# Kernel optimization log

Hardware: AMD Instinct MI355X
Metric: run time of the kernel (lower is better)

The kernel has to match this reference:

```python
import jax, jax.numpy as jnp
import numpy as np

N = 50000
E = 800000
D_IN = 256
HID = 64
HEADS = 4
OUT = 86
EPS_BN = 1e-5
NEG_SLOPE = 0.2


def setup_inputs() -> dict:
    key = jax.random.key(0)
    ks = jax.random.split(key, 16)
    HC = HEADS * HID
    inp = {
        "x": jax.random.normal(ks[0], (N, D_IN), jnp.float32),
        "edge_index": jax.random.randint(ks[1], (2, E), 0, N, jnp.int64),
        # GATConv 1: in=D_IN, out per head=HID, concat=True
        "W1": jax.random.normal(ks[2], (D_IN, HC), jnp.float32) * (1.0 / np.sqrt(D_IN)),
        "att_src1": jax.random.normal(ks[3], (HEADS, HID), jnp.float32) * 0.1,
        "att_dst1": jax.random.normal(ks[4], (HEADS, HID), jnp.float32) * 0.1,
        "b1": jnp.zeros((HC,), jnp.float32),
        # GATConv 2: in=HC, out per head=HID, concat=False (mean over heads)
        "W2": jax.random.normal(ks[5], (HC, HC), jnp.float32) * (1.0 / np.sqrt(HC)),
        "att_src2": jax.random.normal(ks[6], (HEADS, HID), jnp.float32) * 0.1,
        "att_dst2": jax.random.normal(ks[7], (HEADS, HID), jnp.float32) * 0.1,
        "b2": jnp.zeros((HID,), jnp.float32),
        # BatchNorms
        "g1": jnp.ones((HC,), jnp.float32),
        "be1": jnp.zeros((HC,), jnp.float32),
        "g2": jnp.ones((HID,), jnp.float32),
        "be2": jnp.zeros((HID,), jnp.float32),
        # PReLU (single shared weight, torch default init 0.25)
        "prelu_w": jnp.asarray(0.25, jnp.float32),
        # final Linear
        "fcW": jax.random.normal(ks[8], (HID, OUT), jnp.float32) * (1.0 / np.sqrt(HID)),
        "fcb": jnp.zeros((OUT,), jnp.float32),
    }
    return inp


def _gat_conv(x, src, dst, W, att_src, att_dst, bias, concat):
    # PyG GATConv forward (dropout inactive in eval mode).
    n = x.shape[0]
    H, C = att_src.shape
    h = (x @ W).reshape(n, H, C)                      # [N,H,C]
    a_s = jnp.sum(h * att_src[None], axis=-1)         # [N,H]
    a_d = jnp.sum(h * att_dst[None], axis=-1)         # [N,H]
    logits = jax.nn.leaky_relu(a_s[src] + a_d[dst], NEG_SLOPE)  # [E,H]
    # segment softmax over edges grouped by destination node
    m = jax.ops.segment_max(logits, dst, num_segments=n)        # [N,H]
    e = jnp.exp(logits - m[dst])
    s = jax.ops.segment_sum(e, dst, num_segments=n)             # [N,H]
    alpha = e / (s[dst] + 1e-16)                                # [E,H]
    msg = h[src] * alpha[:, :, None]                            # [E,H,C]
    out = jax.ops.segment_sum(msg, dst, num_segments=n)         # [N,H,C]
    if concat:
        return out.reshape(n, H * C) + bias
    return out.mean(axis=1) + bias


def _batch_norm(x, gamma, beta):
    mu = x.mean(axis=0)
    var = x.var(axis=0)
    return gamma * (x - mu) * jax.lax.rsqrt(var + EPS_BN) + beta


def reference(x, edge_index, W1, att_src1, att_dst1, b1, W2, att_src2, att_dst2, b2,
              g1, be1, g2, be2, prelu_w, fcW, fcb):
    n = x.shape[0]
    # GATConv default add_self_loops=True
    loops = jnp.arange(n, dtype=edge_index.dtype)
    src = jnp.concatenate([edge_index[0], loops])
    dst = jnp.concatenate([edge_index[1], loops])

    h = _gat_conv(x, src, dst, W1, att_src1, att_dst1, b1, concat=True)
    h = _batch_norm(h, g1, be1)
    h = jnp.where(h >= 0, h, prelu_w * h)             # PReLU
    # dropout: identity (eval)
    h = _gat_conv(h, src, dst, W2, att_src2, att_dst2, b2, concat=False)
    h = _batch_norm(h, g2, be2)
    h = jax.nn.elu(h)
    return h @ fcW + fcb
```

## Files before the change

### kernel.cpp

```cpp
#include <hip/hip_runtime.h>
#include <math.h>

#define LEAKY 0.2f

typedef __attribute__((ext_vector_type(8))) short short8;
typedef __attribute__((ext_vector_type(4))) float f32x4;

__device__ __forceinline__ float leaky02(float z) { return z >= 0.f ? z : LEAKY * z; }
__device__ __forceinline__ unsigned short f2bf(float f) {
  unsigned u = __float_as_uint(f);
  unsigned r = u + 0x7fffu + ((u >> 16) & 1u);
  return (unsigned short)(r >> 16);
}
__device__ __forceinline__ float bflo(unsigned u) { return __uint_as_float(u << 16); }
__device__ __forceinline__ float bfhi(unsigned u) { return __uint_as_float(u & 0xffff0000u); }

__global__ void count_kernel(const int* __restrict__ ei, int* __restrict__ cnt, int E, int N) {
  int e = blockIdx.x * 256 + threadIdx.x;
  int EP = E + N;
  if (e >= EP) return;
  int d = (e < E) ? ei[E + e] : (e - E);
  atomicAdd(&cnt[d], 1);
}

__global__ __launch_bounds__(256) void scan1_kernel(const int* __restrict__ cnt,
                                                    int* __restrict__ bsums, int n) {
  int i = blockIdx.x * 256 + threadIdx.x;
  int v = (i < n) ? cnt[i] : 0;
  int lane = threadIdx.x & 63, wv = threadIdx.x >> 6;
#pragma unroll
  for (int off = 32; off; off >>= 1) v += __shfl_xor(v, off);
  __shared__ int w[4];
  if (lane == 0) w[wv] = v;
  __syncthreads();
  if (threadIdx.x == 0) bsums[blockIdx.x] = w[0] + w[1] + w[2] + w[3];
}

__global__ __launch_bounds__(256) void scan2_kernel(int* __restrict__ bsums, int nb) {
  int tid = threadIdx.x;
  int lane = tid & 63, wv = tid >> 6;
  int v = (tid < nb) ? bsums[tid] : 0;
  int x = v;
#pragma unroll
  for (int off = 1; off < 64; off <<= 1) {
    int t = __shfl_up(x, off);
    if (lane >= off) x += t;
  }
  __shared__ int ws[4];
  if (lane == 63) ws[wv] = x;
  __syncthreads();
  int woff = 0;
#pragma unroll
  for (int w = 0; w < 4; ++w) if (w < wv) woff += ws[w];
  if (tid < nb) bsums[tid] = x + woff - v;
}

__global__ __launch_bounds__(256) void scan3_kernel(const int* __restrict__ cnt,
                                                    const int* __restrict__ boff,
                                                    int* __restrict__ rowptr,
                                                    int* __restrict__ cursor, int n) {
  int i = blockIdx.x * 256 + threadIdx.x;
  int tid = threadIdx.x, lane = tid & 63, wv = tid >> 6;
  int v = (i < n) ? cnt[i] : 0;
  int x = v;
#pragma unroll
  for (int off = 1; off < 64; off <<= 1) {
    int t = __shfl_up(x, off);
    if (lane >= off) x += t;
  }
  __shared__ int ws[4];
  if (lane == 63) ws[wv] = x;
  __syncthreads();
  int woff = 0;
#pragma unroll
  for (int w = 0; w < 4; ++w) if (w < wv) woff += ws[w];
  int incl = x + woff;
  int base = boff[blockIdx.x];
  if (i < n) {
    rowptr[i + 1] = base + incl;
    cursor[i] = base + incl - v;
  }
  if (i == 0) rowptr[0] = 0;
}

__global__ void fill_kernel(const int* __restrict__ ei, int* __restrict__ cursor,
                            int* __restrict__ srcs, int E, int N) {
  int e = blockIdx.x * 256 + threadIdx.x;
  int EP = E + N;
  if (e >= EP) return;
  int s, d;
  if (e < E) { s = ei[e]; d = ei[E + e]; } else { s = e - E; d = s; }
  int slot = atomicAdd(&cursor[d], 1);
  srcs[slot] = s;
}

__global__ void convw_kernel(const float* __restrict__ W1, const float* __restrict__ W2,
                             unsigned short* __restrict__ Wt1, unsigned short* __restrict__ Wt2) {
  int idx = blockIdx.x * 256 + threadIdx.x;
  const float* W;
  unsigned short* Wt;
  if (idx < 65536) { W = W1; Wt = Wt1; } else { W = W2; Wt = Wt2; idx -= 65536; }
  int c = idx >> 8, k = idx & 255;
  Wt[c * 256 + k] = f2bf(W[k * 256 + c]);
}

template <bool BF16A>
__global__ __launch_bounds__(512) void gemm_kernel(const void* __restrict__ Av,
                                                   const unsigned short* __restrict__ Wt,
                                                   unsigned short* __restrict__ Hout, int M,
                                                   const float* __restrict__ bnsc,
                                                   const float* __restrict__ bnsh,
                                                   const float* __restrict__ pwp,
                                                   const float* __restrict__ att_s,
                                                   const float* __restrict__ att_d,
                                                   float* __restrict__ as_o,
                                                   float* __restrict__ ad_o) {
  __shared__ unsigned short As[128][40];
  __shared__ unsigned short Bs[256][40];
  int tid = threadIdx.x;
  int bm = blockIdx.x * 128;
  int l = tid & 63, wv = tid >> 6;
  int wm = wv >> 2, wn = wv & 3;
  int lr = l & 15, lk = l >> 4;
  f32x4 acc[4][4] = {};
  float pws = pwp ? pwp[0] : 0.f;

  for (int k0 = 0; k0 < 256; k0 += 32) {
#pragma unroll
    for (int it = 0; it < 2; ++it) {
      int i = tid + it * 512;
      int row = i >> 3, kk = (i & 7) * 4;
      int gr = bm + row;
      float v0, v1, v2, v3;
      if (BF16A) {
        uint2 u = make_uint2(0, 0);
        if (gr < M) u = *(const uint2*)((const unsigned short*)Av + (size_t)gr * 256 + k0 + kk);
        v0 = bflo(u.x); v1 = bfhi(u.x); v2 = bflo(u.y); v3 = bfhi(u.y);
      } else {
        float4 va = make_float4(0.f, 0.f, 0.f, 0.f);
        if (gr < M) va = *(const float4*)((const float*)Av + (size_t)gr * 256 + k0 + kk);
        v0 = va.x; v1 = va.y; v2 = va.z; v3 = va.w;
      }
      if (bnsc) {
        float4 sc = *(const float4*)&bnsc[k0 + kk];
        float4 sh = *(const float4*)&bnsh[k0 + kk];
        v0 = fmaf(v0, sc.x, sh.x); v1 = fmaf(v1, sc.y, sh.y);
        v2 = fmaf(v2, sc.z, sh.z); v3 = fmaf(v3, sc.w, sh.w);
        v0 = v0 >= 0.f ? v0 : v0 * pws; v1 = v1 >= 0.f ? v1 : v1 * pws;
        v2 = v2 >= 0.f ? v2 : v2 * pws; v3 = v3 >= 0.f ? v3 : v3 * pws;
      }
      ushort4 u4;
      u4.x = f2bf(v0); u4.y = f2bf(v1); u4.z = f2bf(v2); u4.w = f2bf(v3);
      *(ushort4*)&As[row][kk] = u4;
    }
#pragma unroll
    for (int it = 0; it < 4; ++it) {
      int i = tid + it * 512;
      int c = i >> 3, kk = (i & 7) * 4;
      *(ushort4*)&Bs[c][kk] = *(const ushort4*)&Wt[(size_t)c * 256 + k0 + kk];
    }
    __syncthreads();
    short8 af[4], bfr[4];
#pragma unroll
    for (int mt = 0; mt < 4; ++mt) af[mt] = *(const short8*)&As[wm * 64 + mt * 16 + lr][lk * 8];
#pragma unroll
    for (int nt = 0; nt < 4; ++nt) bfr[nt] = *(const short8*)&Bs[wn * 64 + nt * 16 + lr][lk * 8];
#pragma unroll
    for (int mt = 0; mt < 4; ++mt)
#pragma unroll
      for (int nt = 0; nt < 4; ++nt)
        acc[mt][nt] = __builtin_amdgcn_mfma_f32_16x16x32_bf16(af[mt], bfr[nt], acc[mt][nt], 0, 0, 0);
    __syncthreads();
  }
  float asv[4], adv[4];
#pragma unroll
  for (int nt = 0; nt < 4; ++nt) {
    int gc = wn * 64 + nt * 16 + lr;
    asv[nt] = att_s[gc];
    adv[nt] = att_d[gc];
  }
#pragma unroll
  for (int mt = 0; mt < 4; ++mt) {
#pragma unroll
    for (int r = 0; r < 4; ++r) {
      int gr = bm + wm * 64 + mt * 16 + lk * 4 + r;
      float ps = acc[mt][0][r] * asv[0] + acc[mt][1][r] * asv[1] +
                 acc[mt][2][r] * asv[2] + acc[mt][3][r] * asv[3];
      float pd = acc[mt][0][r] * adv[0] + acc[mt][1][r] * adv[1] +
                 acc[mt][2][r] * adv[2] + acc[mt][3][r] * adv[3];
#pragma unroll
      for (int off = 1; off < 16; off <<= 1) {
        ps += __shfl_xor(ps, off);
        pd += __shfl_xor(pd, off);
      }
      if (lr == 0 && gr < M) {
        as_o[gr * 4 + wn] = ps;
        ad_o[gr * 4 + wn] = pd;
      }
      if (gr < M) {
#pragma unroll
        for (int nt = 0; nt < 4; ++nt)
          Hout[(size_t)gr * 256 + wn * 64 + nt * 16 + lr] = f2bf(acc[mt][nt][r]);
      }
    }
  }
}

__global__ __launch_bounds__(256) void agg_kernel(const unsigned short* __restrict__ h,
                                                  const float* __restrict__ as_,
                                                  const float* __restrict__ ad_,
                                                  const int* __restrict__ rowptr,
                                                  const int* __restrict__ srcs,
                                                  const float* __restrict__ bias,
                                                  unsigned short* __restrict__ out_bf,
                                                  float* __restrict__ out_f,
                                                  int N, int concat) {
  int l = threadIdx.x & 63;
  int n = blockIdx.x * 4 + (threadIdx.x >> 6);
  if (n >= N) return;
  int e0 = rowptr[n], e1 = rowptr[n + 1];
  int deg = e1 - e0;
  int hh = l >> 4, le = l & 15;
  float adh = ad_[n * 4 + hh];
  float a0 = 0.f, a1 = 0.f, a2 = 0.f, a3 = 0.f;

  if (deg <= 64) {
    int sidx[4];
    float lg[4];
#pragma unroll
    for (int t = 0; t < 4; ++t) {
      int j = e0 + le + 16 * t;
      if (j < e1) {
        int s = srcs[j];
        sidx[t] = s;
        lg[t] = leaky02(as_[s * 4 + hh] + adh);
      } else {
        sidx[t] = 0;
        lg[t] = -1e30f;
      }
    }
    float mx = fmaxf(fmaxf(lg[0], lg[1]), fmaxf(lg[2], lg[3]));
#pragma unroll
    for (int off = 1; off < 16; off <<= 1) mx = fmaxf(mx, __shfl_xor(mx, off));
    float ex[4];
    float sm = 0.f;
#pragma unroll
    for (int t = 0; t < 4; ++t) {
      ex[t] = (lg[t] > -1e29f) ? __expf(lg[t] - mx) : 0.f;
      sm += ex[t];
    }
#pragma unroll
    for (int off = 1; off < 16; off <<= 1) sm += __shfl_xor(sm, off);
    float inv = 1.f / (sm + 1e-16f);
    int hsel = hh << 4;
#pragma unroll
    for (int t = 0; t < 4; ++t) {
      int base = e0 + 16 * t;
      if (base >= e1) continue;
      int cntc = min(16, e1 - base);
#pragma unroll 4
      for (int q = 0; q < cntc; ++q) {
        int s = __shfl(sidx[t], q);
        float al = __shfl(ex[t], q + hsel) * inv;
        uint2 hv = *(const uint2*)&h[(size_t)s * 256 + l * 4];
        a0 = fmaf(bflo(hv.x), al, a0);
        a1 = fmaf(bfhi(hv.x), al, a1);
        a2 = fmaf(bflo(hv.y), al, a2);
        a3 = fmaf(bfhi(hv.y), al, a3);
      }
    }
  } else {
    float ad4[4] = {ad_[n * 4], ad_[n * 4 + 1], ad_[n * 4 + 2], ad_[n * 4 + 3]};
    float mx[4] = {-1e30f, -1e30f, -1e30f, -1e30f};
    for (int j = e0 + l; j < e1; j += 64) {
      int s = srcs[j];
      float4 av = *(const float4*)&as_[s * 4];
      mx[0] = fmaxf(mx[0], leaky02(av.x + ad4[0]));
      mx[1] = fmaxf(mx[1], leaky02(av.y + ad4[1]));
      mx[2] = fmaxf(mx[2], leaky02(av.z + ad4[2]));
      mx[3] = fmaxf(mx[3], leaky02(av.w + ad4[3]));
    }
#pragma unroll
    for (int off = 32; off; off >>= 1) {
      mx[0] = fmaxf(mx[0], __shfl_xor(mx[0], off));
      mx[1] = fmaxf(mx[1], __shfl_xor(mx[1], off));
      mx[2] = fmaxf(mx[2], __shfl_xor(mx[2], off));
      mx[3] = fmaxf(mx[3], __shfl_xor(mx[3], off));
    }
    float sm[4] = {0.f, 0.f, 0.f, 0.f};
    for (int j = e0 + l; j < e1; j += 64) {
      int s = srcs[j];
      float4 av = *(const float4*)&as_[s * 4];
      sm[0] += __expf(leaky02(av.x + ad4[0]) - mx[0]);
      sm[1] += __expf(leaky02(av.y + ad4[1]) - mx[1]);
      sm[2] += __expf(leaky02(av.z + ad4[2]) - mx[2]);
      sm[3] += __expf(leaky02(av.w + ad4[3]) - mx[3]);
    }
#pragma unroll
    for (int off = 32; off; off >>= 1) {
      sm[0] += __shfl_xor(sm[0], off);
      sm[1] += __shfl_xor(sm[1], off);
      sm[2] += __shfl_xor(sm[2], off);
      sm[3] += __shfl_xor(sm[3], off);
    }
    float mh = hh == 0 ? mx[0] : hh == 1 ? mx[1] : hh == 2 ? mx[2] : mx[3];
    float sh = hh == 0 ? sm[0] : hh == 1 ? sm[1] : hh == 2 ? sm[2] : sm[3];
    float inv = 1.f / (sh + 1e-16f);
    int j = e0;
    for (; j + 2 <= e1; j += 2) {
      int s0 = srcs[j], s1 = srcs[j + 1];
      float x0 = as_[s0 * 4 + hh], x1 = as_[s1 * 4 + hh];
      uint2 h0 = *(const uint2*)&h[(size_t)s0 * 256 + l * 4];
      uint2 h1 = *(const uint2*)&h[(size_t)s1 * 256 + l * 4];
      float al0 = __expf(leaky02(x0 + adh) - mh) * inv;
      float al1 = __expf(leaky02(x1 + adh) - mh) * inv;
      a0 = fmaf(bflo(h0.x), al0, a0); a1 = fmaf(bfhi(h0.x), al0, a1);
      a2 = fmaf(bflo(h0.y), al0, a2); a3 = fmaf(bfhi(h0.y), al0, a3);
      a0 = fmaf(bflo(h1.x), al1, a0); a1 = fmaf(bfhi(h1.x), al1, a1);
      a2 = fmaf(bflo(h1.y), al1, a2); a3 = fmaf(bfhi(h1.y), al1, a3);
    }
    for (; j < e1; ++j) {
      int s = srcs[j];
      float al = __expf(leaky02(as_[s * 4 + hh] + adh) - mh) * inv;
      uint2 hv = *(const uint2*)&h[(size_t)s * 256 + l * 4];
      a0 = fmaf(bflo(hv.x), al, a0); a1 = fmaf(bfhi(hv.x), al, a1);
      a2 = fmaf(bflo(hv.y), al, a2); a3 = fmaf(bfhi(hv.y), al, a3);
    }
  }

  if (concat) {
    float4 b4 = *(const float4*)&bias[l * 4];
    ushort4 o;
    o.x = f2bf(a0 + b4.x); o.y = f2bf(a1 + b4.y);
    o.z = f2bf(a2 + b4.z); o.w = f2bf(a3 + b4.w);
    *(ushort4*)&out_bf[(size_t)n * 256 + l * 4] = o;
  } else {
    a0 += __shfl_xor(a0, 16); a0 += __shfl_xor(a0, 32);
    a1 += __shfl_xor(a1, 16); a1 += __shfl_xor(a1, 32);
    a2 += __shfl_xor(a2, 16); a2 += __shfl_xor(a2, 32);
    a3 += __shfl_xor(a3, 16); a3 += __shfl_xor(a3, 32);
    if (l < 16) {
      float4 b4 = *(const float4*)&bias[l * 4];
      float4 o = make_float4(0.25f * a0 + b4.x, 0.25f * a1 + b4.y,
                             0.25f * a2 + b4.z, 0.25f * a3 + b4.w);
      *(float4*)&out_f[(size_t)n * 64 + l * 4] = o;
    }
  }
}

__global__ __launch_bounds__(256) void bnstats_bf16_kernel(const unsigned short* __restrict__ x,
                                                           float* __restrict__ sum,
                                                           float* __restrict__ ss, int N) {
  int tid = threadIdx.x;
  int c = (tid & 127) * 2;
  int r = blockIdx.x * 2 + (tid >> 7);
  int stride = gridDim.x * 2;
  float a0 = 0.f, b0 = 0.f, a1 = 0.f, b1 = 0.f;
  for (; r < N; r += stride) {
    unsigned u = *(const unsigned*)&x[(size_t)r * 256 + c];
    float v0 = bflo(u), v1 = bfhi(u);
    a0 += v0; b0 += v0 * v0;
    a1 += v1; b1 += v1 * v1;
  }
  atomicAdd(&sum[c], a0); atomicAdd(&ss[c], b0);
  atomicAdd(&sum[c + 1], a1); atomicAdd(&ss[c + 1], b1);
}

__global__ __launch_bounds__(256) void bnstats_kernel(const float* __restrict__ x,
                                                      float* __restrict__ sum, float* __restrict__ ss,
                                                      int N, int C) {
  int tid = threadIdx.x;
  int f = tid % C;
  int rpb = 256 / C;
  int r = blockIdx.x * rpb + tid / C;
  int stride = gridDim.x * rpb;
  float a = 0.f, b = 0.f;
  for (; r < N; r += stride) {
    float v = x[(size_t)r * C + f];
    a += v;
    b += v * v;
  }
  atomicAdd(&sum[f], a);
  atomicAdd(&ss[f], b);
}

__global__ void bnfinalize_kernel(const float* __restrict__ sum, const float* __restrict__ ss,
                                  const float* __restrict__ gamma, const float* __restrict__ beta,
                                  float* __restrict__ scale, float* __restrict__ shift, int N, int C) {
  int f = threadIdx.x;
  if (f >= C) return;
  float mu = sum[f] / (float)N;
  float var = ss[f] / (float)N - mu * mu;
  float sc = gamma[f] * rsqrtf(var + 1e-5f);
  scale[f] = sc;
  shift[f] = beta[f] - mu * sc;
}

__global__ __launch_bounds__(256) void fc_kernel(const float* __restrict__ x,
                                                 const float* __restrict__ sc, const float* __restrict__ sh,
                                                 const float* __restrict__ W, const float* __restrict__ b,
                                                 float* __restrict__ out, int N) {
  __shared__ float ws[64 * 86];
  __shared__ float xs[32 * 64];
  int tid = threadIdx.x;
  for (int i = tid; i < 64 * 86; i += 256) ws[i] = W[i];
  int n0 = blockIdx.x * 32;
  for (int i = tid; i < 32 * 64; i += 256) {
    int n = n0 + (i >> 6), c = i & 63;
    float v = (n < N) ? x[(size_t)n * 64 + c] : 0.f;
    v = fmaf(v, sc[c], sh[c]);
    xs[i] = v > 0.f ? v : expm1f(v);
  }
  __syncthreads();
  for (int idx = tid; idx < 32 * 86; idx += 256) {
    int nl = idx / 86, o = idx % 86;
    int n = n0 + nl;
    if (n >= N) continue;
    float acc = b[o];
    const float* xr = &xs[nl * 64];
#pragma unroll 8
    for (int k = 0; k < 64; ++k) acc = fmaf(xr[k], ws[k * 86 + o], acc);
    out[(size_t)n * 86 + o] = acc;
  }
}

extern "C" void kernel_launch(void* const* d_in, const int* in_sizes, int n_in,
                              void* d_out, int out_size, void* d_ws, size_t ws_size,
                              hipStream_t stream) {
  const float* x    = (const float*)d_in[0];
  const int*   ei   = (const int*)d_in[1];
  const float* W1   = (const float*)d_in[2];
  const float* asw1 = (const float*)d_in[3];
  const float* adw1 = (const float*)d_in[4];
  const float* b1   = (const float*)d_in[5];
  const float* W2   = (const float*)d_in[6];
  const float* asw2 = (const float*)d_in[7];
  const float* adw2 = (const float*)d_in[8];
  const float* b2   = (const float*)d_in[9];
  const float* g1   = (const float*)d_in[10];
  const float* be1  = (const float*)d_in[11];
  const float* g2   = (const float*)d_in[12];
  const float* be2  = (const float*)d_in[13];
  const float* pw   = (const float*)d_in[14];
  const float* fcW  = (const float*)d_in[15];
  const float* fcb  = (const float*)d_in[16];

  const int N = in_sizes[0] / 256;
  const int E = in_sizes[1] / 2;
  const int EP = E + N;

  char* ws = (char*)d_ws;
  size_t off = 0;
  auto alloc = [&](size_t bytes) {
    char* p = ws + off;
    off += (bytes + 255) & ~(size_t)255;
    return p;
  };
  unsigned short* h    = (unsigned short*)alloc((size_t)N * 256 * 2);
  unsigned short* outb = (unsigned short*)alloc((size_t)N * 256 * 2);
  float* xm   = (float*)alloc((size_t)N * 64 * 4);
  float* as1  = (float*)alloc((size_t)N * 4 * 4);
  float* ad1  = (float*)alloc((size_t)N * 4 * 4);
  float* as2  = (float*)alloc((size_t)N * 4 * 4);
  float* ad2  = (float*)alloc((size_t)N * 4 * 4);
  int* rowptr = (int*)alloc((size_t)(N + 1) * 4);
  int* cnt    = (int*)alloc((size_t)N * 4);
  int* cursor = (int*)alloc((size_t)N * 4);
  int* srcs   = (int*)alloc((size_t)EP * 4);
  int* bsums  = (int*)alloc(1024 * 4);
  unsigned short* Wt1 = (unsigned short*)alloc(65536 * 2);
  unsigned short* Wt2 = (unsigned short*)alloc(65536 * 2);
  float* bstat = (float*)alloc(512 * 4);
  float* bsum = bstat, *bss = bstat + 256;
  float* bsc  = (float*)alloc(256 * 4);
  float* bsh  = (float*)alloc(256 * 4);
  float* bsc2 = (float*)alloc(64 * 4);
  float* bsh2 = (float*)alloc(64 * 4);

  int egrid = (EP + 255) / 256;
  int ngrid4 = (N + 3) / 4;
  int nb = (N + 255) / 256;
  int ggrid = (N + 127) / 128;

  hipMemsetAsync(cnt, 0, (size_t)N * 4, stream);
  count_kernel<<<egrid, 256, 0, stream>>>(ei, cnt, E, N);
  convw_kernel<<<512, 256, 0, stream>>>(W1, W2, Wt1, Wt2);
  scan1_kernel<<<nb, 256, 0, stream>>>(cnt, bsums, N);
  scan2_kernel<<<1, 256, 0, stream>>>(bsums, nb);
  scan3_kernel<<<nb, 256, 0, stream>>>(cnt, bsums, rowptr, cursor, N);
  fill_kernel<<<egrid, 256, 0, stream>>>(ei, cursor, srcs, E, N);

  gemm_kernel<false><<<ggrid, 512, 0, stream>>>(x, Wt1, h, N, nullptr, nullptr, nullptr,
                                                asw1, adw1, as1, ad1);
  agg_kernel<<<ngrid4, 256, 0, stream>>>(h, as1, ad1, rowptr, srcs, b1, outb, nullptr, N, 1);

  hipMemsetAsync(bstat, 0, 512 * 4, stream);
  bnstats_bf16_kernel<<<512, 256, 0, stream>>>(outb, bsum, bss, N);
  bnfinalize_kernel<<<1, 256, 0, stream>>>(bsum, bss, g1, be1, bsc, bsh, N, 256);

  gemm_kernel<true><<<ggrid, 512, 0, stream>>>(outb, Wt2, h, N, bsc, bsh, pw,
                                               asw2, adw2, as2, ad2);
  agg_kernel<<<ngrid4, 256, 0, stream>>>(h, as2, ad2, rowptr, srcs, b2, nullptr, xm, N, 0);

  hipMemsetAsync(bstat, 0, 128 * 4, stream);
  bnstats_kernel<<<512, 256, 0, stream>>>(xm, bstat, bstat + 64, N, 64);
  bnfinalize_kernel<<<1, 64, 0, stream>>>(bstat, bstat + 64, g2, be2, bsc2, bsh2, N, 64);

  fc_kernel<<<(N + 31) / 32, 256, 0, stream>>>(xm, bsc2, bsh2, fcW, fcb, (float*)d_out, N);
}
```

Baseline: 607.8 us.

## Pre-convert x to bf16, shrink GEMM tile to 64 rows, widen aggregation loads

Adds a kernel that converts x to bf16 up front, so the first GEMM reads bf16 like the second one. The GEMM template is removed and the kernel now uses 256-thread blocks with 64-row tiles, each wave covering a 64-column strip across all rows. The aggregation fast path (degree at most 64) processes two edges at once per wave half with 16-byte loads of 8 bf16 values, then combines the halves with shuffles. The cost is an extra pass over x and reloading W once per smaller tile.

```diff
diff --git a/kernel.cpp b/kernel.cpp
--- a/kernel.cpp
+++ b/kernel.cpp
@@ -104,8 +104,20 @@
   Wt[c * 256 + k] = f2bf(W[k * 256 + c]);
 }
 
-template <bool BF16A>
-__global__ __launch_bounds__(512) void gemm_kernel(const void* __restrict__ Av,
+__global__ void convx_kernel(const float* __restrict__ x, unsigned short* __restrict__ xb,
+                             int total) {
+  int i = blockIdx.x * 256 + threadIdx.x;
+  if (i * 8 >= total) return;
+  float4 a = *(const float4*)&x[i * 8];
+  float4 b = *(const float4*)&x[i * 8 + 4];
+  ushort4 u0, u1;
+  u0.x = f2bf(a.x); u0.y = f2bf(a.y); u0.z = f2bf(a.z); u0.w = f2bf(a.w);
+  u1.x = f2bf(b.x); u1.y = f2bf(b.y); u1.z = f2bf(b.z); u1.w = f2bf(b.w);
+  *(ushort4*)&xb[i * 8] = u0;
+  *(ushort4*)&xb[i * 8 + 4] = u1;
+}
+
+__global__ __launch_bounds__(256) void gemm_kernel(const unsigned short* __restrict__ Ab,
                                                    const unsigned short* __restrict__ Wt,
                                                    unsigned short* __restrict__ Hout, int M,
                                                    const float* __restrict__ bnsc,
@@ -115,56 +127,52 @@
                                                    const float* __restrict__ att_d,
                                                    float* __restrict__ as_o,
                                                    float* __restrict__ ad_o) {
-  __shared__ unsigned short As[128][40];
+  __shared__ unsigned short As[64][40];
   __shared__ unsigned short Bs[256][40];
   int tid = threadIdx.x;
-  int bm = blockIdx.x * 128;
+  int bm = blockIdx.x * 64;
   int l = tid & 63, wv = tid >> 6;
-  int wm = wv >> 2, wn = wv & 3;
   int lr = l & 15, lk = l >> 4;
   f32x4 acc[4][4] = {};
+  bool hasbn = (bnsc != nullptr);
   float pws = pwp ? pwp[0] : 0.f;
 
   for (int k0 = 0; k0 < 256; k0 += 32) {
 #pragma unroll
     for (int it = 0; it < 2; ++it) {
-      int i = tid + it * 512;
+      int i = tid + it * 256;
       int row = i >> 3, kk = (i & 7) * 4;
       int gr = bm + row;
-      float v0, v1, v2, v3;
-      if (BF16A) {
-        uint2 u = make_uint2(0, 0);
-        if (gr < M) u = *(const uint2*)((const unsigned short*)Av + (size_t)gr * 256 + k0 + kk);
-        v0 = bflo(u.x); v1 = bfhi(u.x); v2 = bflo(u.y); v3 = bfhi(u.y);
-      } else {
-        float4 va = make_float4(0.f, 0.f, 0.f, 0.f);
-        if (gr < M) va = *(const float4*)((const float*)Av + (size_t)gr * 256 + k0 + kk);
-        v0 = va.x; v1 = va.y; v2 = va.z; v3 = va.w;
-      }
-      if (bnsc) {
+      uint2 u = make_uint2(0, 0);
+      if (gr < M) u = *(const uint2*)&Ab[(size_t)gr * 256 + k0 + kk];
+      if (hasbn) {
         float4 sc = *(const float4*)&bnsc[k0 + kk];
         float4 sh = *(const float4*)&bnsh[k0 + kk];
-        v0 = fmaf(v0, sc.x, sh.x); v1 = fmaf(v1, sc.y, sh.y);
-        v2 = fmaf(v2, sc.z, sh.z); v3 = fmaf(v3, sc.w, sh.w);
+        float v0 = fmaf(bflo(u.x), sc.x, sh.x);
+        float v1 = fmaf(bfhi(u.x), sc.y, sh.y);
+        float v2 = fmaf(bflo(u.y), sc.z, sh.z);
+        float v3 = fmaf(bfhi(u.y), sc.w, sh.w);
         v0 = v0 >= 0.f ? v0 : v0 * pws; v1 = v1 >= 0.f ? v1 : v1 * pws;
         v2 = v2 >= 0.f ? v2 : v2 * pws; v3 = v3 >= 0.f ? v3 : v3 * pws;
-      }
-      ushort4 u4;
-      u4.x = f2bf(v0); u4.y = f2bf(v1); u4.z = f2bf(v2); u4.w = f2bf(v3);
-      *(ushort4*)&As[row][kk] = u4;
-    }
-#pragma unroll
-    for (int it = 0; it < 4; ++it) {
-      int i = tid + it * 512;
+        ushort4 o;
+        o.x = f2bf(v0); o.y = f2bf(v1); o.z = f2bf(v2); o.w = f2bf(v3);
+        *(ushort4*)&As[row][kk] = o;
+      } else {
+        *(uint2*)&As[row][kk] = u;
+      }
+    }
+#pragma unroll
+    for (int it = 0; it < 8; ++it) {
+      int i = tid + it * 256;
       int c = i >> 3, kk = (i & 7) * 4;
-      *(ushort4*)&Bs[c][kk] = *(const ushort4*)&Wt[(size_t)c * 256 + k0 + kk];
+      *(uint2*)&Bs[c][kk] = *(const uint2*)&Wt[(size_t)c * 256 + k0 + kk];
     }
     __syncthreads();
     short8 af[4], bfr[4];
 #pragma unroll
-    for (int mt = 0; mt < 4; ++mt) af[mt] = *(const short8*)&As[wm * 64 + mt * 16 + lr][lk * 8];
-#pragma unroll
-    for (int nt = 0; nt < 4; ++nt) bfr[nt] = *(const short8*)&Bs[wn * 64 + nt * 16 + lr][lk * 8];
+    for (int mt = 0; mt < 4; ++mt) af[mt] = *(const short8*)&As[mt * 16 + lr][lk * 8];
+#pragma unroll
+    for (int nt = 0; nt < 4; ++nt) bfr[nt] = *(const short8*)&Bs[wv * 64 + nt * 16 + lr][lk * 8];
 #pragma unroll
     for (int mt = 0; mt < 4; ++mt)
 #pragma unroll
@@ -175,7 +183,7 @@
   float asv[4], adv[4];
 #pragma unroll
   for (int nt = 0; nt < 4; ++nt) {
-    int gc = wn * 64 + nt * 16 + lr;
+    int gc = wv * 64 + nt * 16 + lr;
     asv[nt] = att_s[gc];
     adv[nt] = att_d[gc];
   }
@@ -183,7 +191,7 @@
   for (int mt = 0; mt < 4; ++mt) {
 #pragma unroll
     for (int r = 0; r < 4; ++r) {
-      int gr = bm + wm * 64 + mt * 16 + lk * 4 + r;
+      int gr = bm + mt * 16 + lk * 4 + r;
       float ps = acc[mt][0][r] * asv[0] + acc[mt][1][r] * asv[1] +
                  acc[mt][2][r] * asv[2] + acc[mt][3][r] * asv[3];
       float pd = acc[mt][0][r] * adv[0] + acc[mt][1][r] * adv[1] +
@@ -194,13 +202,13 @@
         pd += __shfl_xor(pd, off);
       }
       if (lr == 0 && gr < M) {
-        as_o[gr * 4 + wn] = ps;
-        ad_o[gr * 4 + wn] = pd;
+        as_o[gr * 4 + wv] = ps;
+        ad_o[gr * 4 + wv] = pd;
       }
       if (gr < M) {
 #pragma unroll
         for (int nt = 0; nt < 4; ++nt)
-          Hout[(size_t)gr * 256 + wn * 64 + nt * 16 + lr] = f2bf(acc[mt][nt][r]);
+          Hout[(size_t)gr * 256 + wv * 64 + nt * 16 + lr] = f2bf(acc[mt][nt][r]);
       }
     }
   }
@@ -222,7 +230,6 @@
   int deg = e1 - e0;
   int hh = l >> 4, le = l & 15;
   float adh = ad_[n * 4 + hh];
-  float a0 = 0.f, a1 = 0.f, a2 = 0.f, a3 = 0.f;
 
   if (deg <= 64) {
     int sidx[4];
@@ -252,21 +259,61 @@
 #pragma unroll
     for (int off = 1; off < 16; off <<= 1) sm += __shfl_xor(sm, off);
     float inv = 1.f / (sm + 1e-16f);
-    int hsel = hh << 4;
+
+    int p = l >> 5, m = l & 31;
+    int hb = m >> 3;
+    float invb = __shfl(inv, hb << 4);
+    float a[8] = {0.f, 0.f, 0.f, 0.f, 0.f, 0.f, 0.f, 0.f};
 #pragma unroll
     for (int t = 0; t < 4; ++t) {
       int base = e0 + 16 * t;
-      if (base >= e1) continue;
+      if (base >= e1) break;
       int cntc = min(16, e1 - base);
-#pragma unroll 4
-      for (int q = 0; q < cntc; ++q) {
+      int npr = (cntc + 1) >> 1;
+      for (int pr = 0; pr < npr; ++pr) {
+        int q = 2 * pr + p;
         int s = __shfl(sidx[t], q);
-        float al = __shfl(ex[t], q + hsel) * inv;
-        uint2 hv = *(const uint2*)&h[(size_t)s * 256 + l * 4];
-        a0 = fmaf(bflo(hv.x), al, a0);
-        a1 = fmaf(bfhi(hv.x), al, a1);
-        a2 = fmaf(bflo(hv.y), al, a2);
-        a3 = fmaf(bfhi(hv.y), al, a3);
+        float al = __shfl(ex[t], q + (hb << 4)) * invb;
+        uint4 hv = *(const uint4*)&h[(size_t)s * 256 + m * 8];
+        a[0] = fmaf(bflo(hv.x), al, a[0]);
+        a[1] = fmaf(bfhi(hv.x), al, a[1]);
+        a[2] = fmaf(bflo(hv.y), al, a[2]);
+        a[3] = fmaf(bfhi(hv.y), al, a[3]);
+        a[4] = fmaf(bflo(hv.z), al, a[4]);
+        a[5] = fmaf(bfhi(hv.z), al, a[5]);
+        a[6] = fmaf(bflo(hv.w), al, a[6]);
+        a[7] = fmaf(bfhi(hv.w), al, a[7]);
+      }
+    }
+#pragma unroll
+    for (int i = 0; i < 8; ++i) a[i] += __shfl_xor(a[i], 32);
+    if (concat) {
+      if (l < 32) {
+        float4 b0 = *(const float4*)&bias[m * 8];
+        float4 b1 = *(const float4*)&bias[m * 8 + 4];
+        ushort4 o0, o1;
+        o0.x = f2bf(a[0] + b0.x); o0.y = f2bf(a[1] + b0.y);
+        o0.z = f2bf(a[2] + b0.z); o0.w = f2bf(a[3] + b0.w);
+        o1.x = f2bf(a[4] + b1.x); o1.y = f2bf(a[5] + b1.y);
+        o1.z = f2bf(a[6] + b1.z); o1.w = f2bf(a[7] + b1.w);
+        *(ushort4*)&out_bf[(size_t)n * 256 + m * 8] = o0;
+        *(ushort4*)&out_bf[(size_t)n * 256 + m * 8 + 4] = o1;
+      }
+    } else {
+#pragma unroll
+      for (int i = 0; i < 8; ++i) {
+        a[i] += __shfl_xor(a[i], 8);
+        a[i] += __shfl_xor(a[i], 16);
+      }
+      if (l < 8) {
+        float4 b0 = *(const float4*)&bias[m * 8];
+        float4 b1 = *(const float4*)&bias[m * 8 + 4];
+        float4 o0 = make_float4(0.25f * a[0] + b0.x, 0.25f * a[1] + b0.y,
+                                0.25f * a[2] + b0.z, 0.25f * a[3] + b0.w);
+        float4 o1 = make_float4(0.25f * a[4] + b1.x, 0.25f * a[5] + b1.y,
+                                0.25f * a[6] + b1.z, 0.25f * a[7] + b1.w);
+        *(float4*)&out_f[(size_t)n * 64 + m * 8] = o0;
+        *(float4*)&out_f[(size_t)n * 64 + m * 8 + 4] = o1;
       }
     }
   } else {
@@ -306,44 +353,31 @@
     float mh = hh == 0 ? mx[0] : hh == 1 ? mx[1] : hh == 2 ? mx[2] : mx[3];
     float sh = hh == 0 ? sm[0] : hh == 1 ? sm[1] : hh == 2 ? sm[2] : sm[3];
     float inv = 1.f / (sh + 1e-16f);
-    int j = e0;
-    for (; j + 2 <= e1; j += 2) {
-      int s0 = srcs[j], s1 = srcs[j + 1];
-      float x0 = as_[s0 * 4 + hh], x1 = as_[s1 * 4 + hh];
-      uint2 h0 = *(const uint2*)&h[(size_t)s0 * 256 + l * 4];
-      uint2 h1 = *(const uint2*)&h[(size_t)s1 * 256 + l * 4];
-      float al0 = __expf(leaky02(x0 + adh) - mh) * inv;
-      float al1 = __expf(leaky02(x1 + adh) - mh) * inv;
-      a0 = fmaf(bflo(h0.x), al0, a0); a1 = fmaf(bfhi(h0.x), al0, a1);
-      a2 = fmaf(bflo(h0.y), al0, a2); a3 = fmaf(bfhi(h0.y), al0, a3);
-      a0 = fmaf(bflo(h1.x), al1, a0); a1 = fmaf(bfhi(h1.x), al1, a1);
-      a2 = fmaf(bflo(h1.y), al1, a2); a3 = fmaf(bfhi(h1.y), al1, a3);
-    }
-    for (; j < e1; ++j) {
+    float a0 = 0.f, a1 = 0.f, a2 = 0.f, a3 = 0.f;
+    for (int j = e0; j < e1; ++j) {
       int s = srcs[j];
       float al = __expf(leaky02(as_[s * 4 + hh] + adh) - mh) * inv;
       uint2 hv = *(const uint2*)&h[(size_t)s * 256 + l * 4];
       a0 = fmaf(bflo(hv.x), al, a0); a1 = fmaf(bfhi(hv.x), al, a1);
       a2 = fmaf(bflo(hv.y), al, a2); a3 = fmaf(bfhi(hv.y), al, a3);
     }
-  }
-
-  if (concat) {
-    float4 b4 = *(const float4*)&bias[l * 4];
-    ushort4 o;
-    o.x = f2bf(a0 + b4.x); o.y = f2bf(a1 + b4.y);
-    o.z = f2bf(a2 + b4.z); o.w = f2bf(a3 + b4.w);
-    *(ushort4*)&out_bf[(size_t)n * 256 + l * 4] = o;
-  } else {
-    a0 += __shfl_xor(a0, 16); a0 += __shfl_xor(a0, 32);
-    a1 += __shfl_xor(a1, 16); a1 += __shfl_xor(a1, 32);
-    a2 += __shfl_xor(a2, 16); a2 += __shfl_xor(a2, 32);
-    a3 += __shfl_xor(a3, 16); a3 += __shfl_xor(a3, 32);
-    if (l < 16) {
+    if (concat) {
       float4 b4 = *(const float4*)&bias[l * 4];
-      float4 o = make_float4(0.25f * a0 + b4.x, 0.25f * a1 + b4.y,
-                             0.25f * a2 + b4.z, 0.25f * a3 + b4.w);
-      *(float4*)&out_f[(size_t)n * 64 + l * 4] = o;
+      ushort4 o;
+      o.x = f2bf(a0 + b4.x); o.y = f2bf(a1 + b4.y);
+      o.z = f2bf(a2 + b4.z); o.w = f2bf(a3 + b4.w);
+      *(ushort4*)&out_bf[(size_t)n * 256 + l * 4] = o;
+    } else {
+      a0 += __shfl_xor(a0, 16); a0 += __shfl_xor(a0, 32);
+      a1 += __shfl_xor(a1, 16); a1 += __shfl_xor(a1, 32);
+      a2 += __shfl_xor(a2, 16); a2 += __shfl_xor(a2, 32);
+      a3 += __shfl_xor(a3, 16); a3 += __shfl_xor(a3, 32);
+      if (l < 16) {
+        float4 b4 = *(const float4*)&bias[l * 4];
+        float4 o = make_float4(0.25f * a0 + b4.x, 0.25f * a1 + b4.y,
+                               0.25f * a2 + b4.z, 0.25f * a3 + b4.w);
+        *(float4*)&out_f[(size_t)n * 64 + l * 4] = o;
+      }
     }
   }
 }
@@ -456,6 +490,7 @@
     off += (bytes + 255) & ~(size_t)255;
     return p;
   };
+  unsigned short* xb   = (unsigned short*)alloc((size_t)N * 256 * 2);
   unsigned short* h    = (unsigned short*)alloc((size_t)N * 256 * 2);
   unsigned short* outb = (unsigned short*)alloc((size_t)N * 256 * 2);
   float* xm   = (float*)alloc((size_t)N * 64 * 4);
@@ -480,26 +515,27 @@
   int egrid = (EP + 255) / 256;
   int ngrid4 = (N + 3) / 4;
   int nb = (N + 255) / 256;
-  int ggrid = (N + 127) / 128;
+  int ggrid = (N + 63) / 64;
 
   hipMemsetAsync(cnt, 0, (size_t)N * 4, stream);
   count_kernel<<<egrid, 256, 0, stream>>>(ei, cnt, E, N);
   convw_kernel<<<512, 256, 0, stream>>>(W1, W2, Wt1, Wt2);
+  convx_kernel<<<(N * 32 + 255) / 256, 256, 0, stream>>>(x, xb, N * 256);
   scan1_kernel<<<nb, 256, 0, stream>>>(cnt, bsums, N);
   scan2_kernel<<<1, 256, 0, stream>>>(bsums, nb);
   scan3_kernel<<<nb, 256, 0, stream>>>(cnt, bsums, rowptr, cursor, N);
   fill_kernel<<<egrid, 256, 0, stream>>>(ei, cursor, srcs, E, N);
 
-  gemm_kernel<false><<<ggrid, 512, 0, stream>>>(x, Wt1, h, N, nullptr, nullptr, nullptr,
-                                                asw1, adw1, as1, ad1);
+  gemm_kernel<<<ggrid, 256, 0, stream>>>(xb, Wt1, h, N, nullptr, nullptr, nullptr,
+                                         asw1, adw1, as1, ad1);
   agg_kernel<<<ngrid4, 256, 0, stream>>>(h, as1, ad1, rowptr, srcs, b1, outb, nullptr, N, 1);
 
   hipMemsetAsync(bstat, 0, 512 * 4, stream);
   bnstats_bf16_kernel<<<512, 256, 0, stream>>>(outb, bsum, bss, N);
   bnfinalize_kernel<<<1, 256, 0, stream>>>(bsum, bss, g1, be1, bsc, bsh, N, 256);
 
-  gemm_kernel<true><<<ggrid, 512, 0, stream>>>(outb, Wt2, h, N, bsc, bsh, pw,
-                                               asw2, adw2, as2, ad2);
+  gemm_kernel<<<ggrid, 256, 0, stream>>>(outb, Wt2, h, N, bsc, bsh, pw,
+                                         asw2, adw2, as2, ad2);
   agg_kernel<<<ngrid4, 256, 0, stream>>>(h, as2, ad2, rowptr, srcs, b2, nullptr, xm, N, 0);
 
   hipMemsetAsync(bstat, 0, 128 * 4, stream);
```

Measured after the change: 586.4 us. -3.5%, faster.
